# Performance work log

Measured on AMD Instinct MI355X. Metric: run time of the kernel, lower is better.

Reference implementation:

```python
import jax, jax.numpy as jnp
import numpy as np

N_POS = 8192          # number of positive samples
N_NEG = 4000          # negatives per positive
N_TOT = N_POS + N_POS * N_NEG


def setup_inputs() -> dict:
    key = jax.random.key(0)
    k1, k2 = jax.random.split(key)
    predict_val = jax.random.normal(k1, (N_TOT,), dtype=jnp.float32)
    # 'index' is a permutation; the module reorders predict_val by argsort(index)
    index = jax.random.permutation(k2, jnp.arange(N_TOT, dtype=jnp.int64))
    return {"predict_val": predict_val, "index": index, "num": N_NEG, "num_pos": N_POS}


def reference(predict_val, index, num, num_pos):
    # index_tuple = sorted(enumerate(index)) by value -> reorder by argsort(index)
    pv = predict_val[jnp.argsort(index)]
    pos = pv[:num_pos]                                  # [num_pos]
    neg = pv[num_pos:num_pos + num_pos * num]
    neg = neg.reshape(num_pos, num)                     # [num_pos, num]
    # rank of pos among {neg, pos} sorted descending == 1 + #(neg > pos)
    # (ties are randomly broken in the original; measure-zero for continuous scores)
    rank = 1 + jnp.sum(neg > pos[:, None], axis=-1)     # [num_pos], int
    sample_mrr = 1.0 / rank.astype(pv.dtype)            # [num_pos]
    mrr = jnp.mean(sample_mrr)
    return mrr, sample_mrr
```

## Files before the change

### kernel.cpp

```cpp
#include <hip/hip_runtime.h>


constexpr int N_POS = 8192;
constexpr int N_NEG = 4000;

__global__ __launch_bounds__(256) void scatter_pos_kernel(
    const int4* __restrict__ idx4, const float* __restrict__ pv,
    float* __restrict__ pos, int nvec) {
  int stride = gridDim.x * blockDim.x;
  for (int j = blockIdx.x * blockDim.x + threadIdx.x; j < nvec; j += stride) {
    int4 v = idx4[j];
    if (v.x < N_POS) pos[v.x] = pv[4 * j + 0];
    if (v.y < N_POS) pos[v.y] = pv[4 * j + 1];
    if (v.z < N_POS) pos[v.z] = pv[4 * j + 2];
    if (v.w < N_POS) pos[v.w] = pv[4 * j + 3];
  }
}

__global__ __launch_bounds__(1024) void count_kernel(
    const int4* __restrict__ idx4, const float4* __restrict__ pv4,
    const float* __restrict__ pos, unsigned long long* __restrict__ cnt,
    int nvec) {
  __shared__ float pos_lds[N_POS];
  __shared__ unsigned lcnt[N_POS / 2];
  for (int i = threadIdx.x; i < N_POS; i += blockDim.x) pos_lds[i] = pos[i];
  for (int i = threadIdx.x; i < N_POS / 2; i += blockDim.x) lcnt[i] = 0u;
  __syncthreads();

  int stride = gridDim.x * blockDim.x;
  for (int j = blockIdx.x * blockDim.x + threadIdx.x; j < nvec; j += stride) {
    int4 v = idx4[j];
    float4 x = pv4[j];
#define DO_ELEM(IV, XV)                                                  \
    if ((IV) >= N_POS) {                                                 \
      unsigned r = (unsigned)((IV) - N_POS) / (unsigned)N_NEG;           \
      if ((XV) > pos_lds[r])                                             \
        atomicAdd(&lcnt[r >> 1], 1u << ((r & 1u) * 16u));                \
    }
    DO_ELEM(v.x, x.x)
    DO_ELEM(v.y, x.y)
    DO_ELEM(v.z, x.z)
    DO_ELEM(v.w, x.w)
#undef DO_ELEM
  }
  __syncthreads();

  for (int s = threadIdx.x; s < N_POS / 4; s += blockDim.x) {
    unsigned long long lo = lcnt[2 * s];
    unsigned long long hi = lcnt[2 * s + 1];
    unsigned long long p = lo | (hi << 32);
    if (p) atomicAdd(&cnt[s], p);
  }
}

__global__ __launch_bounds__(1024) void finalize_kernel(
    const unsigned long long* __restrict__ cnt, float* __restrict__ out) {
  __shared__ float wsum[16];
  int t = threadIdx.x;
  float s = 0.f;
  for (int k = 0; k < 2; ++k) {
    unsigned long long p = cnt[2 * t + k];
    int base = 8 * t + 4 * k;
#pragma unroll
    for (int e = 0; e < 4; ++e) {
      unsigned c = (unsigned)(p >> (16 * e)) & 0xFFFFu;
      float m = 1.0f / (float)(1u + c);
      out[1 + base + e] = m;
      s += m;
    }
  }
#pragma unroll
  for (int off = 32; off > 0; off >>= 1) s += __shfl_down(s, off, 64);
  if ((t & 63) == 0) wsum[t >> 6] = s;
  __syncthreads();
  if (t < 64) {
    float v = (t < 16) ? wsum[t] : 0.f;
#pragma unroll
    for (int off = 8; off > 0; off >>= 1) v += __shfl_down(v, off, 64);
    if (t == 0) out[0] = v / (float)N_POS;
  }
}

extern "C" void kernel_launch(void* const* d_in, const int* in_sizes, int n_in,
                              void* d_out, int out_size, void* d_ws, size_t ws_size,
                              hipStream_t stream) {
  const float* pv = (const float*)d_in[0];
  const int* idx = (const int*)d_in[1];
  float* out = (float*)d_out;

  float* pos = (float*)d_ws;
  unsigned long long* cnt =
      (unsigned long long*)((char*)d_ws + (size_t)N_POS * sizeof(float));

  int n = in_sizes[0];
  int nvec = n / 4;

  hipMemsetAsync(cnt, 0, (size_t)N_POS * 2, stream);

  scatter_pos_kernel<<<2048, 256, 0, stream>>>((const int4*)idx, pv, pos, nvec);
  count_kernel<<<512, 1024, 0, stream>>>((const int4*)idx, (const float4*)pv,
                                         pos, cnt, nvec);
  finalize_kernel<<<1, 1024, 0, stream>>>(cnt, out);
}
```

Before: 288.7 us.

## Replace global atomics with per-block count slab and parallel reduce kernel

Each count block now writes its packed 16-bit counters to its own slab slice instead of doing global 64-bit atomics, and a 16-block reduce kernel sums the slabs and computes the MRR outputs, accumulating the mean with a float atomicAdd. Streaming loads now use nontemporal hints and the grid-stride loops are unrolled by two, so more loads are in flight. The LDS counters are unpacked to one u32 per position, which removes the packed shift-add. This trades atomic contention for a 512x2048 u64 slab write and read, plus an extra memset of the output scalar.

```diff
diff --git a/kernel.cpp b/kernel.cpp
--- a/kernel.cpp
+++ b/kernel.cpp
@@ -3,81 +3,118 @@
 
 constexpr int N_POS = 8192;
 constexpr int N_NEG = 4000;
+constexpr int CNT_BLOCKS = 512;
+constexpr int NSLOT = N_POS / 4;
+
+typedef int   vint4   __attribute__((ext_vector_type(4)));
+typedef float vfloat4 __attribute__((ext_vector_type(4)));
+typedef unsigned int  u32;
+typedef unsigned long long u64;
 
 __global__ __launch_bounds__(256) void scatter_pos_kernel(
-    const int4* __restrict__ idx4, const float* __restrict__ pv,
+    const vint4* __restrict__ idx4, const float* __restrict__ pv,
     float* __restrict__ pos, int nvec) {
-  int stride = gridDim.x * blockDim.x;
-  for (int j = blockIdx.x * blockDim.x + threadIdx.x; j < nvec; j += stride) {
-    int4 v = idx4[j];
-    if (v.x < N_POS) pos[v.x] = pv[4 * j + 0];
-    if (v.y < N_POS) pos[v.y] = pv[4 * j + 1];
-    if (v.z < N_POS) pos[v.z] = pv[4 * j + 2];
-    if (v.w < N_POS) pos[v.w] = pv[4 * j + 3];
+  const int stride = gridDim.x * blockDim.x;
+  int j = blockIdx.x * blockDim.x + threadIdx.x;
+#define SC_ELEM(V, JJ)                                   \
+  if ((V).x < N_POS) pos[(V).x] = pv[4 * (JJ) + 0];      \
+  if ((V).y < N_POS) pos[(V).y] = pv[4 * (JJ) + 1];      \
+  if ((V).z < N_POS) pos[(V).z] = pv[4 * (JJ) + 2];      \
+  if ((V).w < N_POS) pos[(V).w] = pv[4 * (JJ) + 3];
+  for (; j + stride < nvec; j += 2 * stride) {
+    vint4 a = __builtin_nontemporal_load(&idx4[j]);
+    vint4 b = __builtin_nontemporal_load(&idx4[j + stride]);
+    SC_ELEM(a, j)
+    SC_ELEM(b, j + stride)
+  }
+  for (; j < nvec; j += stride) {
+    vint4 a = __builtin_nontemporal_load(&idx4[j]);
+    SC_ELEM(a, j)
+  }
+#undef SC_ELEM
+}
+
+__global__ __launch_bounds__(1024) void count_kernel(
+    const vint4* __restrict__ idx4, const vfloat4* __restrict__ pv4,
+    const float* __restrict__ pos, u64* __restrict__ slab, int nvec) {
+  __shared__ float pos_lds[N_POS];
+  __shared__ u32 lcnt[N_POS];
+  for (int i = threadIdx.x; i < N_POS; i += 1024) {
+    pos_lds[i] = pos[i];
+    lcnt[i] = 0u;
+  }
+  __syncthreads();
+
+  const int stride = gridDim.x * blockDim.x;
+  int j = blockIdx.x * blockDim.x + threadIdx.x;
+#define CT_ELEM(IV, XV)                                              \
+  if ((IV) >= N_POS) {                                               \
+    unsigned r = (unsigned)((IV) - N_POS) / (unsigned)N_NEG;         \
+    if ((XV) > pos_lds[r]) atomicAdd(&lcnt[r], 1u);                  \
+  }
+#define CT_VEC(V, X)                                                 \
+  CT_ELEM((V).x, (X).x) CT_ELEM((V).y, (X).y)                        \
+  CT_ELEM((V).z, (X).z) CT_ELEM((V).w, (X).w)
+  for (; j + stride < nvec; j += 2 * stride) {
+    vint4 va = __builtin_nontemporal_load(&idx4[j]);
+    vint4 vb = __builtin_nontemporal_load(&idx4[j + stride]);
+    vfloat4 xa = __builtin_nontemporal_load(&pv4[j]);
+    vfloat4 xb = __builtin_nontemporal_load(&pv4[j + stride]);
+    CT_VEC(va, xa)
+    CT_VEC(vb, xb)
+  }
+  for (; j < nvec; j += stride) {
+    vint4 va = __builtin_nontemporal_load(&idx4[j]);
+    vfloat4 xa = __builtin_nontemporal_load(&pv4[j]);
+    CT_VEC(va, xa)
+  }
+#undef CT_VEC
+#undef CT_ELEM
+  __syncthreads();
+
+  u64* my = slab + (size_t)blockIdx.x * NSLOT;
+  const uint4* lq = (const uint4*)lcnt;
+  for (int s = threadIdx.x; s < NSLOT; s += 1024) {
+    uint4 q = lq[s];
+    u64 p = (u64)(q.x & 0xFFFFu) | ((u64)(q.y & 0xFFFFu) << 16) |
+            ((u64)(q.z & 0xFFFFu) << 32) | ((u64)(q.w & 0xFFFFu) << 48);
+    __builtin_nontemporal_store(p, &my[s]);
   }
 }
 
-__global__ __launch_bounds__(1024) void count_kernel(
-    const int4* __restrict__ idx4, const float4* __restrict__ pv4,
-    const float* __restrict__ pos, unsigned long long* __restrict__ cnt,
-    int nvec) {
-  __shared__ float pos_lds[N_POS];
-  __shared__ unsigned lcnt[N_POS / 2];
-  for (int i = threadIdx.x; i < N_POS; i += blockDim.x) pos_lds[i] = pos[i];
-  for (int i = threadIdx.x; i < N_POS / 2; i += blockDim.x) lcnt[i] = 0u;
-  __syncthreads();
+__global__ __launch_bounds__(1024) void reduce_kernel(
+    const u64* __restrict__ slab, float* __restrict__ out) {
+  int k = blockIdx.x * 1024 + threadIdx.x;
+  int slot = k >> 3, part = k & 7;
+  u64 acc = 0;
+  const u64* base = slab + (size_t)(part * 64) * NSLOT + slot;
+#pragma unroll 8
+  for (int b = 0; b < 64; ++b) acc += base[(size_t)b * NSLOT];
+  acc += __shfl_down(acc, 4, 64);
+  acc += __shfl_down(acc, 2, 64);
+  acc += __shfl_down(acc, 1, 64);
 
-  int stride = gridDim.x * blockDim.x;
-  for (int j = blockIdx.x * blockDim.x + threadIdx.x; j < nvec; j += stride) {
-    int4 v = idx4[j];
-    float4 x = pv4[j];
-#define DO_ELEM(IV, XV)                                                  \
-    if ((IV) >= N_POS) {                                                 \
-      unsigned r = (unsigned)((IV) - N_POS) / (unsigned)N_NEG;           \
-      if ((XV) > pos_lds[r])                                             \
-        atomicAdd(&lcnt[r >> 1], 1u << ((r & 1u) * 16u));                \
-    }
-    DO_ELEM(v.x, x.x)
-    DO_ELEM(v.y, x.y)
-    DO_ELEM(v.z, x.z)
-    DO_ELEM(v.w, x.w)
-#undef DO_ELEM
+  float lsum = 0.f;
+  if (part == 0) {
+    float m0 = 1.0f / (float)(1u + (u32)(acc & 0xFFFFu));
+    float m1 = 1.0f / (float)(1u + (u32)((acc >> 16) & 0xFFFFu));
+    float m2 = 1.0f / (float)(1u + (u32)((acc >> 32) & 0xFFFFu));
+    float m3 = 1.0f / (float)(1u + (u32)((acc >> 48) & 0xFFFFu));
+    vfloat4 m = {m0, m1, m2, m3};
+    *(vfloat4*)&out[1 + 4 * slot] = m;
+    lsum = m0 + m1 + m2 + m3;
   }
-  __syncthreads();
-
-  for (int s = threadIdx.x; s < N_POS / 4; s += blockDim.x) {
-    unsigned long long lo = lcnt[2 * s];
-    unsigned long long hi = lcnt[2 * s + 1];
-    unsigned long long p = lo | (hi << 32);
-    if (p) atomicAdd(&cnt[s], p);
-  }
-}
-
-__global__ __launch_bounds__(1024) void finalize_kernel(
-    const unsigned long long* __restrict__ cnt, float* __restrict__ out) {
   __shared__ float wsum[16];
+#pragma unroll
+  for (int off = 32; off > 0; off >>= 1) lsum += __shfl_down(lsum, off, 64);
   int t = threadIdx.x;
-  float s = 0.f;
-  for (int k = 0; k < 2; ++k) {
-    unsigned long long p = cnt[2 * t + k];
-    int base = 8 * t + 4 * k;
-#pragma unroll
-    for (int e = 0; e < 4; ++e) {
-      unsigned c = (unsigned)(p >> (16 * e)) & 0xFFFFu;
-      float m = 1.0f / (float)(1u + c);
-      out[1 + base + e] = m;
-      s += m;
-    }
-  }
-#pragma unroll
-  for (int off = 32; off > 0; off >>= 1) s += __shfl_down(s, off, 64);
-  if ((t & 63) == 0) wsum[t >> 6] = s;
+  if ((t & 63) == 0) wsum[t >> 6] = lsum;
   __syncthreads();
   if (t < 64) {
     float v = (t < 16) ? wsum[t] : 0.f;
 #pragma unroll
     for (int off = 8; off > 0; off >>= 1) v += __shfl_down(v, off, 64);
-    if (t == 0) out[0] = v / (float)N_POS;
+    if (t == 0) atomicAdd(&out[0], v / (float)N_POS);
   }
 }
 
@@ -89,16 +126,15 @@
   float* out = (float*)d_out;
 
   float* pos = (float*)d_ws;
-  unsigned long long* cnt =
-      (unsigned long long*)((char*)d_ws + (size_t)N_POS * sizeof(float));
+  u64* slab = (u64*)((char*)d_ws + 32 * 1024);
 
   int n = in_sizes[0];
   int nvec = n / 4;
 
-  hipMemsetAsync(cnt, 0, (size_t)N_POS * 2, stream);
-
-  scatter_pos_kernel<<<2048, 256, 0, stream>>>((const int4*)idx, pv, pos, nvec);
-  count_kernel<<<512, 1024, 0, stream>>>((const int4*)idx, (const float4*)pv,
-                                         pos, cnt, nvec);
-  finalize_kernel<<<1, 1024, 0, stream>>>(cnt, out);
+  hipMemsetAsync(out, 0, sizeof(float), stream);
+  scatter_pos_kernel<<<2048, 256, 0, stream>>>((const vint4*)idx, pv, pos, nvec);
+  count_kernel<<<CNT_BLOCKS, 1024, 0, stream>>>((const vint4*)idx,
+                                                (const vfloat4*)pv, pos, slab,
+                                                nvec);
+  reduce_kernel<<<16, 1024, 0, stream>>>(slab, out);
 }
```

Measured after the change: 309.2 us. +7.1%, slower.
